# Optimization experiments

Hardware: AMD Instinct MI355X
Metric: run time of the kernel (lower is better)

Reference implementation:

```python
import jax, jax.numpy as jnp
import numpy as np

NUM_HEADS = 12


def setup_inputs() -> dict:
    key = jax.random.key(0)
    ks = jax.random.split(key, 10)
    B, S, H = 4, 1024, 768
    hd = H // NUM_HEADS
    hk = hv = 64
    scale = 1.0 / np.sqrt(H)
    inp = {
        "hidden_states": jax.random.normal(ks[0], (B, S, H), dtype=jnp.float32),
        "attention_mask": jnp.ones((B, S), dtype=jnp.float32),
        "Wq": jax.random.normal(ks[1], (H, H), dtype=jnp.float32) * scale,
        "bq": jnp.zeros((H,), dtype=jnp.float32),
        "Wk": jax.random.normal(ks[2], (H, H), dtype=jnp.float32) * scale,
        "bk": jnp.zeros((H,), dtype=jnp.float32),
        "Wv": jax.random.normal(ks[3], (H, H), dtype=jnp.float32) * scale,
        "bv": jnp.zeros((H,), dtype=jnp.float32),
        "E_key": jax.random.normal(ks[4], (2 * hk + 1, hd), dtype=jnp.float32) * 0.02,
        "E_val": jax.random.normal(ks[5], (2 * hv + 1, hd), dtype=jnp.float32) * 0.02,
    }
    return inp


def reference(hidden_states, attention_mask, Wq, bq, Wk, bk, Wv, bv, E_key, E_val):
    B, S, H = hidden_states.shape
    hd = H // NUM_HEADS

    def split_heads(x):  # [B,S,H] -> [B,nh,S,hd]
        return x.reshape(B, S, NUM_HEADS, hd).transpose(0, 2, 1, 3)

    q = split_heads(hidden_states @ Wq + bq)
    k = split_heads(hidden_states @ Wk + bk)
    v = split_heads(hidden_states @ Wv + bv)

    # content scores (note: original code applies NO 1/sqrt(d) scaling)
    scores = jnp.einsum("bhid,bhjd->bhij", q, k)

    # relative key-position scores: scores_pos[i,j] = q_i . E_key[j-i+hk] (banded)
    Rk = E_key.shape[0]
    hk = (Rk - 1) // 2
    rel = jnp.arange(S)[None, :] - jnp.arange(S)[:, None] + hk  # [S,S]
    valid_k = (rel >= 0) & (rel < Rk)
    p = jnp.einsum("bhid,rd->bhir", q, E_key)  # [B,nh,S,Rk]
    rel_c = jnp.clip(rel, 0, Rk - 1)
    scores_pos = jnp.take_along_axis(p, rel_c[None, None, :, :], axis=-1)
    scores = scores + jnp.where(valid_k[None, None], scores_pos, 0.0)

    # attention mask: (1 - m) * finfo.min added to scores
    ext = (1.0 - attention_mask[:, None, None, :]) * jnp.finfo(scores.dtype).min
    probs = jax.nn.softmax(scores + ext, axis=-1)

    ctx = jnp.einsum("bhij,bhjd->bhid", probs, v)

    # relative value-position: ctx_pos[i] = sum_j probs[i,j] * E_val[j-i+hv]
    Rv = E_val.shape[0]
    hv = (Rv - 1) // 2
    j_idx = jnp.arange(S)[:, None] + jnp.arange(Rv)[None, :] - hv  # [S,Rv]
    valid_v = (j_idx >= 0) & (j_idx < S)
    j_c = jnp.clip(j_idx, 0, S - 1)
    probs_band = jnp.take_along_axis(probs, j_c[None, None, :, :], axis=-1)
    probs_band = probs_band * valid_v[None, None].astype(probs.dtype)
    ctx = ctx + jnp.einsum("bhir,rd->bhid", probs_band, E_val)

    return ctx.transpose(0, 2, 1, 3).reshape(B, S, H)
```

## Files before the change

kernel.cpp:

```cpp
#include <hip/hip_runtime.h>
#include <hip/hip_bf16.h>
#include <math.h>

#define NH 12
#define SEQ 1024
#define HD 64
#define HDIM 768
#define BSZ 4
#define RK 129
#define FMIN -3.4028234663852886e38f
#define LOG2E 1.4426950408889634f

typedef __attribute__((ext_vector_type(8))) short short8;
typedef __attribute__((ext_vector_type(4))) short short4v;
typedef __attribute__((ext_vector_type(2))) unsigned uint2v;
typedef __attribute__((ext_vector_type(8))) _Float16 f16x8;
typedef __attribute__((ext_vector_type(4))) float f32x4;

__device__ inline short f2bf(float x) {
    union { __hip_bfloat16 h; short s; } u;
    u.h = __float2bfloat16(x);
    return u.s;
}
__device__ inline unsigned cvtpk(float lo, float hi) {
    unsigned r;
    asm("v_cvt_pk_bf16_f32 %0, %1, %2" : "=v"(r) : "v"(lo), "v"(hi));
    return r;
}
__device__ inline float fexp2(float x) {
    float r;
    asm("v_exp_f32 %0, %1" : "=v"(r) : "v"(x));
    return r;
}

__device__ inline void async_load16(void* lds, const void* g) {
    __builtin_amdgcn_global_load_lds(
        (const __attribute__((address_space(1))) unsigned int*)g,
        (__attribute__((address_space(3))) unsigned int*)lds, 16, 0, 0);
}

#define BAR()    asm volatile("s_barrier" ::: "memory")
#define WAITV0() asm volatile("s_waitcnt vmcnt(0)" ::: "memory")
#define WAITV2() asm volatile("s_waitcnt vmcnt(2)" ::: "memory")

#define NXCHUNK 393216
#define NECHUNK 1032
#define NEVCHUNK 1280
#define NCONVB ((NXCHUNK + NECHUNK + NEVCHUNK + 255) / 256)
#define NTRB   (144 * 3)
__global__ __launch_bounds__(256) void prep_kernel(
    const float* __restrict__ X, const float* __restrict__ Ek,
    const float* __restrict__ Ev,
    const float* __restrict__ Wq, const float* __restrict__ Wk, const float* __restrict__ Wv,
    _Float16* __restrict__ Xh, _Float16* __restrict__ Ekh, short* __restrict__ Evt,
    _Float16* __restrict__ Wtq, _Float16* __restrict__ Wtk, _Float16* __restrict__ Wtv)
{
    const int bidg = blockIdx.x;
    if (bidg < NCONVB) {
        int idx = bidg * 256 + threadIdx.x;
        if (idx < NXCHUNK + NECHUNK) {
            const float* src;
            _Float16* dst;
            if (idx < NXCHUNK) { src = X; dst = Xh; }
            else { idx -= NXCHUNK; src = Ek; dst = Ekh; }
            float4 a = ((const float4*)src)[idx * 2];
            float4 b = ((const float4*)src)[idx * 2 + 1];
            f16x8 o;
            o[0] = (_Float16)a.x; o[1] = (_Float16)a.y; o[2] = (_Float16)a.z; o[3] = (_Float16)a.w;
            o[4] = (_Float16)b.x; o[5] = (_Float16)b.y; o[6] = (_Float16)b.z; o[7] = (_Float16)b.w;
            ((f16x8*)dst)[idx] = o;
        } else if (idx < NXCHUNK + NECHUNK + NEVCHUNK) {
            idx -= NXCHUNK + NECHUNK;
            const int dim = idx / 20;
            const int r0  = (idx % 20) * 8;
            short8 o;
#pragma unroll
            for (int e = 0; e < 8; ++e) {
                int rel = r0 + e;
                float v = (rel < RK) ? Ev[(size_t)rel * HD + dim] : 0.0f;
                o[e] = f2bf(v);
            }
            *(short8*)&Evt[(size_t)dim * 160 + r0] = o;
        }
        return;
    }
    const int bid2 = bidg - NCONVB;
    const int z = bid2 / 144;
    const int r = bid2 % 144;
    const float* __restrict__ W = (z == 0) ? Wq : (z == 1) ? Wk : Wv;
    _Float16* __restrict__ Wt   = (z == 0) ? Wtq : (z == 1) ? Wtk : Wtv;

    __shared__ float sT[64][65];
    const int t  = threadIdx.x;
    const int k0 = (r / 12) * 64;
    const int n0 = (r % 12) * 64;

    const int c  = (t & 15) * 4;
    const int kr = t >> 4;
#pragma unroll
    for (int rr = 0; rr < 4; ++rr) {
        float4 v = *(const float4*)&W[(size_t)(k0 + kr + rr * 16) * HDIM + n0 + c];
        sT[c + 0][kr + rr * 16] = v.x;
        sT[c + 1][kr + rr * 16] = v.y;
        sT[c + 2][kr + rr * 16] = v.z;
        sT[c + 3][kr + rr * 16] = v.w;
    }
    __syncthreads();
    const int rn = t >> 2;
    const int ck = (t & 3) * 16;
#pragma unroll
    for (int g = 0; g < 2; ++g) {
        f16x8 o;
#pragma unroll
        for (int e = 0; e < 8; ++e) o[e] = (_Float16)sT[rn][ck + g * 8 + e];
        *(f16x8*)&Wt[(size_t)(n0 + rn) * HDIM + k0 + ck + g * 8] = o;
    }
}

__global__ __launch_bounds__(256) void qkv_mfma_kernel(
    const _Float16* __restrict__ Xh,
    const _Float16* __restrict__ Wtq, const _Float16* __restrict__ Wtk, const _Float16* __restrict__ Wtv,
    const float* __restrict__ bq, const float* __restrict__ bk, const float* __restrict__ bv,
    _Float16* __restrict__ Qo, _Float16* __restrict__ Ko, short* __restrict__ Vt)
{
    int bid = blockIdx.x;
    bid = (bid & 7) * 72 + (bid >> 3);
    const int which = bid / 192;
    const int rem   = bid % 192;
    const int n0    = (rem / 32) * 128;
    const int m0    = (rem % 32) * 128;
    const _Float16* __restrict__ Wt = (which == 0) ? Wtq : (which == 1) ? Wtk : Wtv;
    const float* __restrict__ bias  = (which == 0) ? bq : (which == 1) ? bk : bv;
    const float qscale = (which == 0) ? LOG2E : 1.0f;

    __shared__ __align__(16) _Float16 sA[128 * 64];
    __shared__ __align__(16) _Float16 sB[128 * 64];

    const int t  = threadIdx.x;
    const int w  = t >> 6, l = t & 63;
    const int lq = l & 15, lg = l >> 4;
    const int wr = w >> 1, wc = w & 1;

    f32x4 acc[4][4];
#pragma unroll
    for (int i = 0; i < 4; ++i)
#pragma unroll
        for (int j = 0; j < 4; ++j) acc[i][j] = (f32x4){0.f, 0.f, 0.f, 0.f};

    for (int k0 = 0; k0 < HDIM; k0 += 64) {
        __syncthreads();
#pragma unroll
        for (int r = 0; r < 4; ++r) {
            const int cib = r * 256 + w * 64;
            const int ci  = cib + l;
            const int row = ci >> 3, cr = ci & 7;
            const int lc  = cr ^ (row & 7);
            async_load16(&sA[(size_t)cib * 8],
                         &Xh[(size_t)(m0 + row) * HDIM + k0 + lc * 8]);
            async_load16(&sB[(size_t)cib * 8],
                         &Wt[(size_t)(n0 + row) * HDIM + k0 + lc * 8]);
        }
        __syncthreads();

        f16x8 af[4][2], bf[4][2];
#pragma unroll
        for (int i = 0; i < 4; ++i) {
#pragma unroll
            for (int ks = 0; ks < 2; ++ks) {
                int ra = wr * 64 + i * 16 + lq;
                af[i][ks] = *(const f16x8*)((const char*)sA +
                            ra * 128 + ((ks * 64 + lg * 16) ^ ((ra & 7) << 4)));
                int rb = wc * 64 + i * 16 + lq;
                bf[i][ks] = *(const f16x8*)((const char*)sB +
                            rb * 128 + ((ks * 64 + lg * 16) ^ ((rb & 7) << 4)));
            }
        }
#pragma unroll
        for (int i = 0; i < 4; ++i)
#pragma unroll
            for (int j = 0; j < 4; ++j) {
                acc[i][j] = __builtin_amdgcn_mfma_f32_16x16x32_f16(af[i][0], bf[j][0], acc[i][j], 0, 0, 0);
                acc[i][j] = __builtin_amdgcn_mfma_f32_16x16x32_f16(af[i][1], bf[j][1], acc[i][j], 0, 0, 0);
            }
    }

    _Float16* __restrict__ Yh = (which == 0) ? Qo : Ko;
#pragma unroll
    for (int i = 0; i < 4; ++i) {
        const int mb = m0 + wr * 64 + i * 16 + lg * 4;
        const int bb = mb >> 10, ss = mb & 1023;
#pragma unroll
        for (int j = 0; j < 4; ++j) {
            const int n  = n0 + wc * 64 + j * 16 + lq;
            const float bv4 = bias[n];
            const int hh = n >> 6, dd = n & 63;
            if (which == 2) {
                short4v pk;
#pragma unroll
                for (int reg = 0; reg < 4; ++reg)
                    pk[reg] = f2bf(acc[i][j][reg] + bv4);
                *(short4v*)&Vt[((size_t)(bb * NH + hh) * HD + dd) * SEQ + ss] = pk;
            } else {
#pragma unroll
                for (int reg = 0; reg < 4; ++reg) {
                    const size_t off = ((size_t)(bb * NH + hh) * SEQ + ss + reg) * HD + dd;
                    Yh[off] = (_Float16)((acc[i][j][reg] + bv4) * qscale);
                }
            }
        }
    }
}

__global__ __launch_bounds__(256, 3) void attn_mfma_kernel(
    const _Float16* __restrict__ Q, const _Float16* __restrict__ K,
    const short* __restrict__ Vt, const float* __restrict__ mask,
    const _Float16* __restrict__ Ekh, const short* __restrict__ Evt,
    float* __restrict__ out)
{
    __shared__ __align__(16) char smem[50688];
    _Float16* sPpos = (_Float16*)(smem + 29696);
    float*    sMt   = (float*)(smem + 46592);

    int bid = blockIdx.x;
    bid = (bid & 7) * 96 + (bid >> 3);
    const int bh = bid >> 4;
    const int i0 = (bid & 15) * 64;
    const int b  = bh / NH;
    const int h  = bh - b * NH;

    const int t  = threadIdx.x;
    const int w  = t >> 6;
    const int l  = t & 63;
    const int lq = l & 15;
    const int lg = l >> 4;
    const int wrow0 = i0 + w * 16;
    const int bt0 = __builtin_amdgcn_readfirstlane(((wrow0 - 64 + 1024) >> 5) - 32);

    const int krow = t >> 3, klc = (t & 7) ^ (krow & 7);
    const int vrow = t >> 2, vlc = (t & 3) ^ ((vrow >> 1) & 3);
    const _Float16* Ksrc = K + ((size_t)bh * SEQ + krow) * HD + klc * 8;
    const short*    Vsrc = Vt + ((size_t)bh * HD + vrow) * SEQ + vlc * 8;

    async_load16(smem + t * 16,          Ksrc);
    async_load16(smem + 12288 + t * 16,  Vsrc);
    async_load16(smem + 4096 + t * 16,   Ksrc + 32 * HD);
    async_load16(smem + 16384 + t * 16,  Vsrc + 32);

    const _Float16* qp = Q + ((size_t)bh * SEQ + wrow0 + lq) * HD;
    f16x8 qf0 = *(const f16x8*)&qp[lg * 8];
    f16x8 qf1 = *(const f16x8*)&qp[32 + lg * 8];

#pragma unroll
    for (int nt = 0; nt < 9; ++nt) {
        int cc = nt * 16 + lq;
        f16x8 eb0 = {0, 0, 0, 0, 0, 0, 0, 0};
        f16x8 eb1 = {0, 0, 0, 0, 0, 0, 0, 0};
        if (cc < RK) {
            eb0 = *(const f16x8*)&Ekh[(size_t)cc * HD + lg * 8];
            eb1 = *(const f16x8*)&Ekh[(size_t)cc * HD + 32 + lg * 8];
        }
        f32x4 pc = {0.f, 0.f, 0.f, 0.f};
        pc = __builtin_amdgcn_mfma_f32_16x16x32_f16(qf0, eb0, pc, 0, 0, 0);
        pc = __builtin_amdgcn_mfma_f32_16x16x32_f16(qf1, eb1, pc, 0, 0, 0);
        if (cc < RK) {
#pragma unroll
            for (int reg = 0; reg < 4; ++reg)
                sPpos[(w * 16 + lg * 4 + reg) * 132 + cc] = (_Float16)pc[reg];
        }
    }

    {
        float4 mv = *(const float4*)&mask[(size_t)b * SEQ + t * 4];
        float4 mo;
        mo.x = ((1.0f - mv.x) * FMIN) * LOG2E;
        mo.y = ((1.0f - mv.y) * FMIN) * LOG2E;
        mo.z = ((1.0f - mv.z) * FMIN) * LOG2E;
        mo.w = ((1.0f - mv.w) * FMIN) * LOG2E;
        *(float4*)&sMt[t * 4] = mo;
    }

    asm volatile("s_waitcnt vmcnt(2) lgkmcnt(0)" ::: "memory");
    BAR();

    f32x4 acc[4];
#pragma unroll
    for (int nt = 0; nt < 4; ++nt) acc[nt] = (f32x4){0.f, 0.f, 0.f, 0.f};
    f32x4 zacc = {0.f, 0.f, 0.f, 0.f};

    const short8 ones = {0x3F80, 0x3F80, 0x3F80, 0x3F80,
                         0x3F80, 0x3F80, 0x3F80, 0x3F80};

    unsigned band[5][2][2];
#pragma unroll
    for (int s = 0; s < 5; ++s)
#pragma unroll
        for (int ct = 0; ct < 2; ++ct) { band[s][ct][0] = 0u; band[s][ct][1] = 0u; }

    const int ck0 = ((lg ^ (lq & 7)) << 4);
    const int ck1 = (((4 + lg) ^ (lq & 7)) << 4);
    char* sPw = smem + 24576 + w * 1280;
    const int vslot = (lg ^ ((lq >> 1) & 3)) << 4;

    char* bK0 = smem;          char* bK1 = smem + 4096;  char* bK2 = smem + 8192;
    char* bV0 = smem + 12288;  char* bV1 = smem + 16384; char* bV2 = smem + 20480;

    for (int jt = 0; jt < 32; ++jt) {
        const int j0 = jt * 32;

        if (jt < 30) {
            const int jn0 = j0 + 64;
            async_load16(bK2 + t * 16, Ksrc + (size_t)jn0 * HD);
            async_load16(bV2 + t * 16, Vsrc + jn0);
        }

        f32x4 sc[2];
#pragma unroll
        for (int ct = 0; ct < 2; ++ct) {
            const int rb = (ct * 16 + lq) * 128;
            f16x8 kb0 = *(const f16x8*)(bK0 + rb + ck0);
            f16x8 kb1 = *(const f16x8*)(bK0 + rb + ck1);
            f32x4 s = {0.f, 0.f, 0.f, 0.f};
            s = __builtin_amdgcn_mfma_f32_16x16x32_f16(kb0, qf0, s, 0, 0, 0);
            s = __builtin_amdgcn_mfma_f32_16x16x32_f16(kb1, qf1, s, 0, 0, 0);
            sc[ct] = s;
        }

        float p[2][4];
        if ((unsigned)(jt - bt0) < 5u) {
#pragma unroll
            for (int s = 0; s < 5; ++s) {
                if (jt == bt0 + s) {
#pragma unroll
                    for (int ct = 0; ct < 2; ++ct) {
                        const int kbase = j0 + ct * 16 + lg * 4;
                        const int relb  = kbase - wrow0 - lq + 64;
                        f32x4 mtv = *(const f32x4*)&sMt[kbase];
#pragma unroll
                        for (int reg = 0; reg < 4; ++reg) {
                            float sv = sc[ct][reg] + mtv[reg];
                            const int rel = relb + reg;
                            const bool inb = ((unsigned)rel < (unsigned)RK);
                            if (inb) sv += (float)sPpos[(w * 16 + lq) * 132 + rel];
                            p[ct][reg] = fexp2(sv);
                        }
                        band[s][ct][0] = cvtpk(p[ct][0], p[ct][1]);
                        band[s][ct][1] = cvtpk(p[ct][2], p[ct][3]);
                    }
                }
            }
        } else {
#pragma unroll
            for (int ct = 0; ct < 2; ++ct) {
                f32x4 mtv = *(const f32x4*)&sMt[j0 + ct * 16 + lg * 4];
#pragma unroll
                for (int reg = 0; reg < 4; ++reg)
                    p[ct][reg] = fexp2(sc[ct][reg] + mtv[reg]);
            }
        }

#pragma unroll
        for (int ct = 0; ct < 2; ++ct) {
            uint2v pw;
            pw[0] = cvtpk(p[ct][0], p[ct][1]);
            pw[1] = cvtpk(p[ct][2], p[ct][3]);
            *(uint2v*)(sPw + lq * 80 + ct * 32 + lg * 8) = pw;
        }

        short8 pa = *(const short8*)(sPw + lq * 80 + lg * 16);
        zacc = __builtin_amdgcn_mfma_f32_16x16x32_bf16(pa, ones, zacc, 0, 0, 0);

#pragma unroll
        for (int nt = 0; nt < 4; ++nt) {
            short8 vb = *(const short8*)(bV0 + (nt * 16 + lq) * 64 + vslot);
            acc[nt] = __builtin_amdgcn_mfma_f32_16x16x32_bf16(pa, vb, acc[nt], 0, 0, 0);
        }

        if (jt < 30)       WAITV2();
        else if (jt == 30) WAITV0();
        BAR();

        char* tk = bK0; bK0 = bK1; bK1 = bK2; bK2 = tk;
        char* tv = bV0; bV0 = bV1; bV1 = bV2; bV2 = tv;
    }

    char* bandLds = smem + w * 5120;
    {
        short8 z8 = {0, 0, 0, 0, 0, 0, 0, 0};
#pragma unroll
        for (int i = 0; i < 5; ++i)
            *(short8*)(bandLds + l * 16 + i * 1024) = z8;
    }
#pragma unroll
    for (int s = 0; s < 5; ++s) {
        const int jts = bt0 + s;
        if ((unsigned)jts < 32u) {
#pragma unroll
            for (int ct = 0; ct < 2; ++ct)
#pragma unroll
                for (int hh = 0; hh < 2; ++hh) {
                    const unsigned pw = band[s][ct][hh];
                    const int k0v  = jts * 32 + ct * 16 + lg * 4 + hh * 2;
                    const int rel0 = k0v - wrow0 - lq + 64;
                    if ((unsigned)rel0 < (unsigned)RK)
                        *(short*)(bandLds + lq * 320 + rel0 * 2) = (short)(pw & 0xffff);
                    if ((unsigned)(rel0 + 1) < (unsigned)RK)
                        *(short*)(bandLds + lq * 320 + rel0 * 2 + 2) = (short)(pw >> 16);
                }
        }
    }

    short8 bandA[5];
#pragma unroll
    for (int ks = 0; ks < 5; ++ks)
        bandA[ks] = *(const short8*)(bandLds + lq * 320 + ks * 64 + lg * 16);
#pragma unroll
    for (int nt = 0; nt < 4; ++nt) {
#pragma unroll
        for (int ks = 0; ks < 5; ++ks) {
            short8 eb = *(const short8*)&Evt[(size_t)(nt * 16 + lq) * 160 + ks * 32 + lg * 8];
            acc[nt] = __builtin_amdgcn_mfma_f32_16x16x32_bf16(bandA[ks], eb, acc[nt], 0, 0, 0);
        }
    }

#pragma unroll
    for (int nt = 0; nt < 4; ++nt) {
#pragma unroll
        for (int reg = 0; reg < 4; ++reg) {
            int qi = wrow0 + lg * 4 + reg;
            out[((size_t)b * SEQ + qi) * HDIM + h * HD + nt * 16 + lq] =
                acc[nt][reg] / zacc[reg];
        }
    }
}

extern "C" void kernel_launch(void* const* d_in, const int* in_sizes, int n_in,
                              void* d_out, int out_size, void* d_ws, size_t ws_size,
                              hipStream_t stream) {
    const float* X    = (const float*)d_in[0];
    const float* mask = (const float*)d_in[1];
    const float* Wq   = (const float*)d_in[2];
    const float* bq   = (const float*)d_in[3];
    const float* Wk   = (const float*)d_in[4];
    const float* bk   = (const float*)d_in[5];
    const float* Wv   = (const float*)d_in[6];
    const float* bv   = (const float*)d_in[7];
    const float* Ek   = (const float*)d_in[8];
    const float* Ev   = (const float*)d_in[9];
    float* out        = (float*)d_out;

    char* ws = (char*)d_ws;
    const size_t SZ_QKV = (size_t)BSZ * NH * SEQ * HD * 2;
    const size_t SZ_W   = (size_t)HDIM * HDIM * 2;
    _Float16* Qh  = (_Float16*)(ws);
    _Float16* Kh  = (_Float16*)(ws + SZ_QKV);
    short*    Vt  = (short*)   (ws + 2 * SZ_QKV);
    _Float16* Xh  = (_Float16*)(ws + 3 * SZ_QKV);
    _Float16* Wtq = (_Float16*)(ws + 4 * SZ_QKV);
    _Float16* Wtk = (_Float16*)(ws + 4 * SZ_QKV + SZ_W);
    _Float16* Wtv = (_Float16*)(ws + 4 * SZ_QKV + 2 * SZ_W);
    _Float16* Ekh = (_Float16*)(ws + 4 * SZ_QKV + 3 * SZ_W);
    short*    Evt = (short*)   (ws + 4 * SZ_QKV + 3 * SZ_W + 20480);

    prep_kernel<<<NCONVB + NTRB, 256, 0, stream>>>(
        X, Ek, Ev, Wq, Wk, Wv, Xh, Ekh, Evt, Wtq, Wtk, Wtv);
    qkv_mfma_kernel<<<576, 256, 0, stream>>>(Xh, Wtq, Wtk, Wtv, bq, bk, bv, Qh, Kh, Vt);
    attn_mfma_kernel<<<768, 256, 0, stream>>>(Qh, Kh, Vt, mask, Ekh, Evt, out);
}
```

Baseline: 76.52 us.

## Software-pipeline attention loop: compute next tile's scores while doing current PV

Restructures the attention main loop so the QK^T scores and exp/pack of tile jt+1 are computed before the P·V MFMAs of tile jt, with double-buffered per-wave P buffers in LDS. The P buffer layout switches from padded rows to an XOR swizzle, and barrier/wait placement moves to the top of each iteration. This aims to overlap exp/VALU work with MFMA work and cut stalls around the per-tile barrier, at the cost of more LDS (which may reduce occupancy) and a prologue/epilogue.

```diff
diff --git a/kernel.cpp b/kernel.cpp
--- a/kernel.cpp
+++ b/kernel.cpp
@@ -217,9 +217,9 @@
     const _Float16* __restrict__ Ekh, const short* __restrict__ Evt,
     float* __restrict__ out)
 {
-    __shared__ __align__(16) char smem[50688];
-    _Float16* sPpos = (_Float16*)(smem + 29696);
-    float*    sMt   = (float*)(smem + 46592);
+    __shared__ __align__(16) char smem[53760];
+    _Float16* sPpos = (_Float16*)(smem + 32768);
+    float*    sMt   = (float*)(smem + 49664);
 
     int bid = blockIdx.x;
     bid = (bid & 7) * 96 + (bid >> 3);
@@ -279,9 +279,6 @@
         *(float4*)&sMt[t * 4] = mo;
     }
 
-    asm volatile("s_waitcnt vmcnt(2) lgkmcnt(0)" ::: "memory");
-    BAR();
-
     f32x4 acc[4];
 #pragma unroll
     for (int nt = 0; nt < 4; ++nt) acc[nt] = (f32x4){0.f, 0.f, 0.f, 0.f};
@@ -298,49 +295,42 @@
 
     const int ck0 = ((lg ^ (lq & 7)) << 4);
     const int ck1 = (((4 + lg) ^ (lq & 7)) << 4);
-    char* sPw = smem + 24576 + w * 1280;
+    char* sPw = smem + 24576 + w * 1024;
+    const int pswz = (lq & 3) << 4;
     const int vslot = (lg ^ ((lq >> 1) & 3)) << 4;
 
     char* bK0 = smem;          char* bK1 = smem + 4096;  char* bK2 = smem + 8192;
     char* bV0 = smem + 12288;  char* bV1 = smem + 16384; char* bV2 = smem + 20480;
 
-    for (int jt = 0; jt < 32; ++jt) {
-        const int j0 = jt * 32;
-
-        if (jt < 30) {
-            const int jn0 = j0 + 64;
-            async_load16(bK2 + t * 16, Ksrc + (size_t)jn0 * HD);
-            async_load16(bV2 + t * 16, Vsrc + jn0);
-        }
-
+    auto score_pack = [&](int jtc, const char* bKn, char* pbw) {
+        const int j0c = jtc * 32;
         f32x4 sc[2];
 #pragma unroll
         for (int ct = 0; ct < 2; ++ct) {
             const int rb = (ct * 16 + lq) * 128;
-            f16x8 kb0 = *(const f16x8*)(bK0 + rb + ck0);
-            f16x8 kb1 = *(const f16x8*)(bK0 + rb + ck1);
+            f16x8 kb0 = *(const f16x8*)(bKn + rb + ck0);
+            f16x8 kb1 = *(const f16x8*)(bKn + rb + ck1);
             f32x4 s = {0.f, 0.f, 0.f, 0.f};
             s = __builtin_amdgcn_mfma_f32_16x16x32_f16(kb0, qf0, s, 0, 0, 0);
             s = __builtin_amdgcn_mfma_f32_16x16x32_f16(kb1, qf1, s, 0, 0, 0);
             sc[ct] = s;
         }
-
         float p[2][4];
-        if ((unsigned)(jt - bt0) < 5u) {
+        if ((unsigned)(jtc - bt0) < 5u) {
 #pragma unroll
             for (int s = 0; s < 5; ++s) {
-                if (jt == bt0 + s) {
+                if (jtc == bt0 + s) {
 #pragma unroll
                     for (int ct = 0; ct < 2; ++ct) {
-                        const int kbase = j0 + ct * 16 + lg * 4;
+                        const int kbase = j0c + ct * 16 + lg * 4;
                         const int relb  = kbase - wrow0 - lq + 64;
                         f32x4 mtv = *(const f32x4*)&sMt[kbase];
 #pragma unroll
                         for (int reg = 0; reg < 4; ++reg) {
                             float sv = sc[ct][reg] + mtv[reg];
                             const int rel = relb + reg;
-                            const bool inb = ((unsigned)rel < (unsigned)RK);
-                            if (inb) sv += (float)sPpos[(w * 16 + lq) * 132 + rel];
+                            if ((unsigned)rel < (unsigned)RK)
+                                sv += (float)sPpos[(w * 16 + lq) * 132 + rel];
                             p[ct][reg] = fexp2(sv);
                         }
                         band[s][ct][0] = cvtpk(p[ct][0], p[ct][1]);
@@ -351,38 +341,61 @@
         } else {
 #pragma unroll
             for (int ct = 0; ct < 2; ++ct) {
-                f32x4 mtv = *(const f32x4*)&sMt[j0 + ct * 16 + lg * 4];
+                f32x4 mtv = *(const f32x4*)&sMt[j0c + ct * 16 + lg * 4];
 #pragma unroll
                 for (int reg = 0; reg < 4; ++reg)
                     p[ct][reg] = fexp2(sc[ct][reg] + mtv[reg]);
             }
         }
-
 #pragma unroll
         for (int ct = 0; ct < 2; ++ct) {
             uint2v pw;
             pw[0] = cvtpk(p[ct][0], p[ct][1]);
             pw[1] = cvtpk(p[ct][2], p[ct][3]);
-            *(uint2v*)(sPw + lq * 80 + ct * 32 + lg * 8) = pw;
-        }
-
-        short8 pa = *(const short8*)(sPw + lq * 80 + lg * 16);
+            *(uint2v*)(pbw + lq * 64 + ((ct * 32 + lg * 8) ^ pswz)) = pw;
+        }
+    };
+
+    WAITV2();
+    BAR();
+    score_pack(0, bK0, sPw + 0 * 4096);
+
+    for (int jt = 0; jt < 31; ++jt) {
+        WAITV0();
+        BAR();
+        if (jt <= 29) {
+            const int jn0 = jt * 32 + 64;
+            async_load16(bK2 + t * 16, Ksrc + (size_t)jn0 * HD);
+            async_load16(bV2 + t * 16, Vsrc + jn0);
+        }
+
+        score_pack(jt + 1, bK1, sPw + ((jt + 1) & 1) * 4096);
+
+        char* pbw = sPw + (jt & 1) * 4096;
+        short8 pa = *(const short8*)(pbw + lq * 64 + ((lg << 4) ^ pswz));
         zacc = __builtin_amdgcn_mfma_f32_16x16x32_bf16(pa, ones, zacc, 0, 0, 0);
-
 #pragma unroll
         for (int nt = 0; nt < 4; ++nt) {
             short8 vb = *(const short8*)(bV0 + (nt * 16 + lq) * 64 + vslot);
             acc[nt] = __builtin_amdgcn_mfma_f32_16x16x32_bf16(pa, vb, acc[nt], 0, 0, 0);
         }
 
-        if (jt < 30)       WAITV2();
-        else if (jt == 30) WAITV0();
-        BAR();
-
         char* tk = bK0; bK0 = bK1; bK1 = bK2; bK2 = tk;
         char* tv = bV0; bV0 = bV1; bV1 = bV2; bV2 = tv;
     }
 
+    {
+        char* pbw = sPw + (31 & 1) * 4096;
+        short8 pa = *(const short8*)(pbw + lq * 64 + ((lg << 4) ^ pswz));
+        zacc = __builtin_amdgcn_mfma_f32_16x16x32_bf16(pa, ones, zacc, 0, 0, 0);
+#pragma unroll
+        for (int nt = 0; nt < 4; ++nt) {
+            short8 vb = *(const short8*)(bV0 + (nt * 16 + lq) * 64 + vslot);
+            acc[nt] = __builtin_amdgcn_mfma_f32_16x16x32_bf16(pa, vb, acc[nt], 0, 0, 0);
+        }
+    }
+
+    BAR();
     char* bandLds = smem + w * 5120;
     {
         short8 z8 = {0, 0, 0, 0, 0, 0, 0, 0};
```

Measured after the change: 77.00 us. Within noise of the previous version (+0.6%).

## Double subtile per barrier with 4-slot K/V ring and register-held position bias

Applied to the files above, without the earlier changes.

The main attention loop now handles two 32-key subtiles between barriers and uses a 4-slot K/V ring buffer, so barriers and waits drop from 32 to 16. Loads for the next pair are issued before the current pair is computed. The relative-key position scores for each wave's band are read once into registers (ppos) ahead of the loop, replacing per-iteration LDS reads, and the shared P-pos table is overlaid on the K/V buffers, which cuts total LDS. The cost is higher register pressure from the 40-float ppos array and a full vmcnt(0) wait each iteration instead of a partial one, which could limit occupancy or overlap.

```diff
diff --git a/kernel.cpp b/kernel.cpp
--- a/kernel.cpp
+++ b/kernel.cpp
@@ -39,9 +39,10 @@
         (__attribute__((address_space(3))) unsigned int*)lds, 16, 0, 0);
 }
 
-#define BAR()    asm volatile("s_barrier" ::: "memory")
-#define WAITV0() asm volatile("s_waitcnt vmcnt(0)" ::: "memory")
-#define WAITV2() asm volatile("s_waitcnt vmcnt(2)" ::: "memory")
+#define BAR()      asm volatile("s_barrier" ::: "memory")
+#define WAITV0()   asm volatile("s_waitcnt vmcnt(0)" ::: "memory")
+#define WAITLGKM() do { asm volatile("s_waitcnt lgkmcnt(0)" ::: "memory"); \
+                        __builtin_amdgcn_sched_barrier(0); } while (0)
 
 #define NXCHUNK 393216
 #define NECHUNK 1032
@@ -217,9 +218,8 @@
     const _Float16* __restrict__ Ekh, const short* __restrict__ Evt,
     float* __restrict__ out)
 {
-    __shared__ __align__(16) char smem[50688];
-    _Float16* sPpos = (_Float16*)(smem + 29696);
-    float*    sMt   = (float*)(smem + 46592);
+    __shared__ __align__(16) char smem[41984];
+    float* sMt = (float*)(smem + 37888);
 
     int bid = blockIdx.x;
     bid = (bid & 7) * 96 + (bid >> 3);
@@ -241,15 +241,11 @@
     const _Float16* Ksrc = K + ((size_t)bh * SEQ + krow) * HD + klc * 8;
     const short*    Vsrc = Vt + ((size_t)bh * HD + vrow) * SEQ + vlc * 8;
 
-    async_load16(smem + t * 16,          Ksrc);
-    async_load16(smem + 12288 + t * 16,  Vsrc);
-    async_load16(smem + 4096 + t * 16,   Ksrc + 32 * HD);
-    async_load16(smem + 16384 + t * 16,  Vsrc + 32);
-
     const _Float16* qp = Q + ((size_t)bh * SEQ + wrow0 + lq) * HD;
     f16x8 qf0 = *(const f16x8*)&qp[lg * 8];
     f16x8 qf1 = *(const f16x8*)&qp[32 + lg * 8];
 
+    _Float16* povl = (_Float16*)(smem + 16384 + w * 4224);
 #pragma unroll
     for (int nt = 0; nt < 9; ++nt) {
         int cc = nt * 16 + lq;
@@ -265,8 +261,23 @@
         if (cc < RK) {
 #pragma unroll
             for (int reg = 0; reg < 4; ++reg)
-                sPpos[(w * 16 + lg * 4 + reg) * 132 + cc] = (_Float16)pc[reg];
-        }
+                povl[(lg * 4 + reg) * 132 + cc] = (_Float16)pc[reg];
+        }
+    }
+    float ppos[5][2][4];
+#pragma unroll
+    for (int s = 0; s < 5; ++s) {
+        const int jts = bt0 + s;
+#pragma unroll
+        for (int ct = 0; ct < 2; ++ct)
+#pragma unroll
+            for (int reg = 0; reg < 4; ++reg) {
+                const int rel = jts * 32 + ct * 16 + lg * 4 + reg - wrow0 - lq + 64;
+                float v = 0.f;
+                if ((unsigned)jts < 32u && (unsigned)rel < (unsigned)RK)
+                    v = (float)povl[lq * 132 + rel];
+                ppos[s][ct][reg] = v;
+            }
     }
 
     {
@@ -279,7 +290,14 @@
         *(float4*)&sMt[t * 4] = mo;
     }
 
-    asm volatile("s_waitcnt vmcnt(2) lgkmcnt(0)" ::: "memory");
+    WAITLGKM();
+    BAR();
+
+    async_load16(smem + t * 16,          Ksrc);
+    async_load16(smem + 16384 + t * 16,  Vsrc);
+    async_load16(smem + 4096 + t * 16,   Ksrc + 32 * HD);
+    async_load16(smem + 20480 + t * 16,  Vsrc + 32);
+    WAITV0();
     BAR();
 
     f32x4 acc[4];
@@ -298,51 +316,35 @@
 
     const int ck0 = ((lg ^ (lq & 7)) << 4);
     const int ck1 = (((4 + lg) ^ (lq & 7)) << 4);
-    char* sPw = smem + 24576 + w * 1280;
+    char* sPw = smem + 32768 + w * 1280;
     const int vslot = (lg ^ ((lq >> 1) & 3)) << 4;
 
-    char* bK0 = smem;          char* bK1 = smem + 4096;  char* bK2 = smem + 8192;
-    char* bV0 = smem + 12288;  char* bV1 = smem + 16384; char* bV2 = smem + 20480;
-
-    for (int jt = 0; jt < 32; ++jt) {
-        const int j0 = jt * 32;
-
-        if (jt < 30) {
-            const int jn0 = j0 + 64;
-            async_load16(bK2 + t * 16, Ksrc + (size_t)jn0 * HD);
-            async_load16(bV2 + t * 16, Vsrc + jn0);
-        }
-
+    auto do_subtile = [&](int jtc) {
+        char* bK = smem + (jtc & 3) * 4096;
+        char* bV = smem + 16384 + (jtc & 3) * 4096;
+        const int j0c = jtc * 32;
         f32x4 sc[2];
 #pragma unroll
         for (int ct = 0; ct < 2; ++ct) {
             const int rb = (ct * 16 + lq) * 128;
-            f16x8 kb0 = *(const f16x8*)(bK0 + rb + ck0);
-            f16x8 kb1 = *(const f16x8*)(bK0 + rb + ck1);
+            f16x8 kb0 = *(const f16x8*)(bK + rb + ck0);
+            f16x8 kb1 = *(const f16x8*)(bK + rb + ck1);
             f32x4 s = {0.f, 0.f, 0.f, 0.f};
             s = __builtin_amdgcn_mfma_f32_16x16x32_f16(kb0, qf0, s, 0, 0, 0);
             s = __builtin_amdgcn_mfma_f32_16x16x32_f16(kb1, qf1, s, 0, 0, 0);
             sc[ct] = s;
         }
-
         float p[2][4];
-        if ((unsigned)(jt - bt0) < 5u) {
+        if ((unsigned)(jtc - bt0) < 5u) {
 #pragma unroll
             for (int s = 0; s < 5; ++s) {
-                if (jt == bt0 + s) {
+                if (jtc == bt0 + s) {
 #pragma unroll
                     for (int ct = 0; ct < 2; ++ct) {
-                        const int kbase = j0 + ct * 16 + lg * 4;
-                        const int relb  = kbase - wrow0 - lq + 64;
-                        f32x4 mtv = *(const f32x4*)&sMt[kbase];
-#pragma unroll
-                        for (int reg = 0; reg < 4; ++reg) {
-                            float sv = sc[ct][reg] + mtv[reg];
-                            const int rel = relb + reg;
-                            const bool inb = ((unsigned)rel < (unsigned)RK);
-                            if (inb) sv += (float)sPpos[(w * 16 + lq) * 132 + rel];
-                            p[ct][reg] = fexp2(sv);
-                        }
+                        f32x4 mtv = *(const f32x4*)&sMt[j0c + ct * 16 + lg * 4];
+#pragma unroll
+                        for (int reg = 0; reg < 4; ++reg)
+                            p[ct][reg] = fexp2(sc[ct][reg] + mtv[reg] + ppos[s][ct][reg]);
                         band[s][ct][0] = cvtpk(p[ct][0], p[ct][1]);
                         band[s][ct][1] = cvtpk(p[ct][2], p[ct][3]);
                     }
@@ -351,13 +353,12 @@
         } else {
 #pragma unroll
             for (int ct = 0; ct < 2; ++ct) {
-                f32x4 mtv = *(const f32x4*)&sMt[j0 + ct * 16 + lg * 4];
+                f32x4 mtv = *(const f32x4*)&sMt[j0c + ct * 16 + lg * 4];
 #pragma unroll
                 for (int reg = 0; reg < 4; ++reg)
                     p[ct][reg] = fexp2(sc[ct][reg] + mtv[reg]);
             }
         }
-
 #pragma unroll
         for (int ct = 0; ct < 2; ++ct) {
             uint2v pw;
@@ -365,22 +366,33 @@
             pw[1] = cvtpk(p[ct][2], p[ct][3]);
             *(uint2v*)(sPw + lq * 80 + ct * 32 + lg * 8) = pw;
         }
-
         short8 pa = *(const short8*)(sPw + lq * 80 + lg * 16);
         zacc = __builtin_amdgcn_mfma_f32_16x16x32_bf16(pa, ones, zacc, 0, 0, 0);
-
 #pragma unroll
         for (int nt = 0; nt < 4; ++nt) {
-            short8 vb = *(const short8*)(bV0 + (nt * 16 + lq) * 64 + vslot);
+            short8 vb = *(const short8*)(bV + (nt * 16 + lq) * 64 + vslot);
             acc[nt] = __builtin_amdgcn_mfma_f32_16x16x32_bf16(pa, vb, acc[nt], 0, 0, 0);
         }
-
-        if (jt < 30)       WAITV2();
-        else if (jt == 30) WAITV0();
+    };
+
+    for (int j = 0; j < 16; ++j) {
+        if (j < 15) {
+            const int jn = 2 * j + 2;
+            async_load16(smem + (jn & 3) * 4096 + t * 16,
+                         Ksrc + (size_t)jn * 32 * HD);
+            async_load16(smem + 16384 + (jn & 3) * 4096 + t * 16,
+                         Vsrc + jn * 32);
+            async_load16(smem + ((jn + 1) & 3) * 4096 + t * 16,
+                         Ksrc + (size_t)(jn + 1) * 32 * HD);
+            async_load16(smem + 16384 + ((jn + 1) & 3) * 4096 + t * 16,
+                         Vsrc + (jn + 1) * 32);
+        }
+
+        do_subtile(2 * j);
+        do_subtile(2 * j + 1);
+
+        WAITV0();
         BAR();
-
-        char* tk = bK0; bK0 = bK1; bK1 = bK2; bK2 = tk;
-        char* tv = bV0; bV0 = bV1; bV1 = bV2; bV2 = tv;
     }
 
     char* bandLds = smem + w * 5120;
```

Measured after the change: 76.83 us. No clear change (+0.4%).
